# Kernel optimization log

Measured on AMD Instinct MI355X. Metric: run time of the kernel, lower is better.

## Reference

```python
import jax, jax.numpy as jnp
import numpy as np

DIM = 256
NUM_HEADS = 8
REGIONS = [4, 4, 8, 8, 16, 16, 32, 32]  # per-head local window sizes
B, H_IMG, W_IMG = 8, 64, 64


def setup_inputs() -> dict:
    key = jax.random.key(0)
    ks = jax.random.split(key, 6)
    C = DIM
    s = 0.02
    return {
        'x': jax.random.normal(ks[0], (B, H_IMG * W_IMG, C), jnp.float32),
        'Wq': jax.random.normal(ks[1], (C, C), jnp.float32) * s,
        'Wkv': jax.random.normal(ks[2], (C, 2 * C), jnp.float32) * s,
        'Wlkv': jax.random.normal(ks[3], (C, 2 * C), jnp.float32) * s,
        'Wproj': jax.random.normal(ks[4], (C, C), jnp.float32) * s,
        'bproj': jnp.zeros((C,), jnp.float32),
        'H': H_IMG,
        'W': W_IMG,
    }


def _attn(q, k, v, scale):
    # softmax(q k^T * scale) v, batched over leading dims
    a = jax.nn.softmax(jnp.einsum('...qd,...kd->...qk', q, k) * scale, axis=-1)
    return jnp.einsum('...qk,...kd->...qd', a, v)


def reference(x, Wq, Wkv, Wlkv, Wproj, bproj, H, W):
    Bn, N, C = x.shape
    nh = NUM_HEADS
    Ch = C // nh
    scale = Ch ** -0.5
    M = max(REGIONS)

    q = (x @ Wq).reshape(Bn, N, nh, Ch).transpose(0, 2, 1, 3)            # [B,nh,N,Ch]
    kv = (x @ Wkv).reshape(Bn, N, 2, nh, Ch).transpose(2, 0, 3, 1, 4)    # [2,B,nh,N,Ch]
    k, v = kv[0], kv[1]

    head_outs, global_q = [], []
    for i, p in enumerate(REGIONS):
        def patch(a, p=p):  # [B,N,Ch] -> [B,NP,p*p,Ch]
            a = a.reshape(Bn, H // p, p, W // p, p, Ch)
            return a.transpose(0, 1, 3, 2, 4, 5).reshape(Bn, -1, p * p, Ch)
        qp, kp, vp = patch(q[:, i]), patch(k[:, i]), patch(v[:, i])
        # global query: mean over patches -> [B,p,p,Ch], bilinear upsample to [M,M]
        qg = qp.mean(axis=1).reshape(Bn, p, p, Ch)
        if M // p > 1:
            qg = jax.image.resize(qg, (Bn, M, M, Ch), method='bilinear')
        global_q.append(qg.reshape(Bn, M * M, Ch))
        out = _attn(qp, kp, vp, scale)                                    # [B,NP,p*p,Ch]
        head_outs.append(out.reshape(Bn, N, Ch))  # flatten in PATCH order (matches torch code)

    attn_fused = jnp.stack(head_outs, axis=1).transpose(0, 2, 1, 3).reshape(Bn, N, C)
    Q_g = jnp.stack(global_q, axis=1).transpose(0, 2, 1, 3).reshape(Bn, M * M, C)

    # blend: adaptive avg-pool attn_fused to [M,M] (exact pooling since M|H), cross-attend, upsample
    kh, kw = H // M, W // M
    pooled = attn_fused.reshape(Bn, M, kh, M, kw, C).mean(axis=(2, 4)).reshape(Bn, M * M, C)
    kv2 = (pooled @ Wlkv).reshape(Bn, M * M, 2, nh, Ch).transpose(2, 0, 3, 1, 4)
    k2, v2 = kv2[0], kv2[1]
    Qr = Q_g.reshape(Bn, M * M, nh, Ch).transpose(0, 2, 1, 3)             # [B,nh,M^2,Ch]
    gl = _attn(Qr, k2, v2, scale)                                          # [B,nh,M^2,Ch]
    gl = gl.transpose(0, 2, 1, 3).reshape(Bn, M, M, C)
    gl = jax.image.resize(gl, (Bn, H, W, C), method='bilinear').reshape(Bn, N, C)

    return (attn_fused + gl) @ Wproj + bproj
```

## Files before the change

### kernel.cpp

```cpp
#include <hip/hip_runtime.h>
#include <math.h>


typedef __attribute__((ext_vector_type(8))) short bf16x8;
typedef __attribute__((ext_vector_type(4))) short bf16x4;
typedef __attribute__((ext_vector_type(4))) float f32x4;

__device__ inline float bf2f(unsigned short u) {
  union { unsigned int i; float f; } v; v.i = ((unsigned int)u) << 16; return v.f;
}
__device__ inline unsigned short f2bf(float x) {
  union { float f; unsigned int i; } v; v.f = x;
  return (unsigned short)((v.i + 0x7FFFu + ((v.i >> 16) & 1u)) >> 16);
}

__global__ __launch_bounds__(256) void msa_xcast_r13(
    const float* __restrict__ x, unsigned short* __restrict__ xb)
{
  const size_t i = ((size_t)blockIdx.x * 256 + threadIdx.x) * 8;
  const float4 v0 = *reinterpret_cast<const float4*>(&x[i]);
  const float4 v1 = *reinterpret_cast<const float4*>(&x[i + 4]);
  bf16x8 o;
  o[0] = (short)f2bf(v0.x); o[1] = (short)f2bf(v0.y);
  o[2] = (short)f2bf(v0.z); o[3] = (short)f2bf(v0.w);
  o[4] = (short)f2bf(v1.x); o[5] = (short)f2bf(v1.y);
  o[6] = (short)f2bf(v1.z); o[7] = (short)f2bf(v1.w);
  *reinterpret_cast<bf16x8*>(&xb[i]) = o;
}

__global__ __launch_bounds__(256) void msa_wcast_r13(
    const float* __restrict__ Wq, const float* __restrict__ Wkv,
    const float* __restrict__ Wlkv, const float* __restrict__ Wproj,
    unsigned short* __restrict__ Wqkvt, unsigned short* __restrict__ Wlkvt,
    unsigned short* __restrict__ Wprjt)
{
  const int id = blockIdx.x * 256 + threadIdx.x;
  if (id < 196608) {
    const int r = id >> 8, k = id & 255;
    const float v = (r < 256) ? Wq[(size_t)k * 256 + r] : Wkv[(size_t)k * 512 + (r - 256)];
    Wqkvt[id] = f2bf(v);
  } else if (id < 327680) {
    const int j = id - 196608;
    const int n = j >> 8, k = j & 255;
    Wlkvt[j] = f2bf(Wlkv[(size_t)k * 512 + n]);
  } else if (id < 393216) {
    const int j = id - 327680;
    const int n = j >> 8, k = j & 255;
    Wprjt[j] = f2bf(Wproj[(size_t)k * 256 + n]);
  }
}

__global__ __launch_bounds__(256) void msa_gemm_mfma_r13(
    const unsigned short* __restrict__ Ab, const unsigned short* __restrict__ Wt,
    const float* __restrict__ bias, float* __restrict__ Cf,
    unsigned short* __restrict__ Cb, int K, int N)
{
  __shared__ __align__(16) unsigned short A_lds[128][40];
  __shared__ __align__(16) unsigned short B_lds[128][40];

  const int tid = threadIdx.x;
  const int wave = tid >> 6, lane = tid & 63;
  const int l15 = lane & 15, g = lane >> 4;
  const int bm = blockIdx.y * 128, bn = blockIdx.x * 128;
  const int wr = (wave >> 1) * 64, wc = (wave & 1) * 64;

  f32x4 acc[4][4] = {};

  for (int k0 = 0; k0 < K; k0 += 32) {
    __syncthreads();
#pragma unroll
    for (int s = 0; s < 2; ++s) {
      const int id = tid + s * 256;
      const int row = id >> 2, sg = (id & 3) << 3;
      *reinterpret_cast<bf16x8*>(&A_lds[row][sg]) =
          *reinterpret_cast<const bf16x8*>(&Ab[(size_t)(bm + row) * K + k0 + sg]);
      *reinterpret_cast<bf16x8*>(&B_lds[row][sg]) =
          *reinterpret_cast<const bf16x8*>(&Wt[(size_t)(bn + row) * K + k0 + sg]);
    }
    __syncthreads();

    bf16x8 a_frag[4], b_frag[4];
#pragma unroll
    for (int mi = 0; mi < 4; ++mi)
      a_frag[mi] = *reinterpret_cast<const bf16x8*>(&A_lds[wr + mi * 16 + l15][g << 3]);
#pragma unroll
    for (int ni = 0; ni < 4; ++ni)
      b_frag[ni] = *reinterpret_cast<const bf16x8*>(&B_lds[wc + ni * 16 + l15][g << 3]);
#pragma unroll
    for (int mi = 0; mi < 4; ++mi)
#pragma unroll
      for (int ni = 0; ni < 4; ++ni)
        acc[mi][ni] = __builtin_amdgcn_mfma_f32_16x16x32_bf16(
            a_frag[mi], b_frag[ni], acc[mi][ni], 0, 0, 0);
  }

#pragma unroll
  for (int mi = 0; mi < 4; ++mi)
#pragma unroll
    for (int ni = 0; ni < 4; ++ni) {
      const int col = bn + wc + ni * 16 + l15;
#pragma unroll
      for (int i = 0; i < 4; ++i) {
        const int row = bm + wr + mi * 16 + g * 4 + i;
        float v = acc[mi][ni][i];
        if (bias) v += bias[col];
        const size_t idx = (size_t)row * N + col;
        if (Cb) Cb[idx] = f2bf(v); else Cf[idx] = v;
      }
    }
}

__global__ __launch_bounds__(256) void msa_attn_mfma_r13(
    const unsigned short* __restrict__ qsrc, const unsigned short* __restrict__ kvsrc,
    float* __restrict__ outf, unsigned short* __restrict__ outb, int mode)
{
  __shared__ __align__(16) unsigned short K_lds[64][40];
  __shared__ __align__(16) unsigned short V_lds[32][68];

  const int tid = threadIdx.x;
  const int wave = tid >> 6, lane = tid & 63;
  const int q16 = lane & 15, h = lane >> 4;
  const int b = blockIdx.y;

  int head, NTOK, P2, lp, pm1, base, qstr, kvstr, kofs, vofs;
  if (mode) {
    head = blockIdx.z; NTOK = 1024; P2 = 1024; lp = 0; pm1 = 0; base = 0;
    qstr = 256; kvstr = 512; kofs = 0; vofs = 256;
  } else {
    head = 2 + blockIdx.z;
    lp = (head < 4) ? 3 : (head < 6) ? 4 : 5;
    const int p = 1 << lp; pm1 = p - 1;
    NTOK = 4096; P2 = p * p;
    const int patch = (blockIdx.x * 64) >> (2 * lp);
    const int nbp = 64 >> lp;
    const int hb = patch / nbp, wb = patch - (patch / nbp) * nbp;
    base = ((hb << lp)) * 64 + (wb << lp);
    qstr = 768; kvstr = 768; kofs = 256; vofs = 512;
  }
  const int nq = blockIdx.x * 64 + wave * 16 + q16;
  int n;
  if (mode) n = nq;
  else { const int t = nq & (P2 - 1); n = base + ((t >> lp) << 6) + (t & pm1); }

  const bf16x8 qfrag = *reinterpret_cast<const bf16x8*>(
      qsrc + ((size_t)b * NTOK + n) * qstr + head * 32 + 8 * h);

  const float CEXP = 0.25503485947f;
  float l = 0.f;
  f32x4 o0 = {0.f, 0.f, 0.f, 0.f}, o1 = {0.f, 0.f, 0.f, 0.f};
  const f32x4 zc = {0.f, 0.f, 0.f, 0.f};

  const int skey = tid >> 2;
  const int sh = tid & 3;

  for (int kc = 0; kc < P2; kc += 64) {
    __syncthreads();
    {
      const int kk = kc + skey;
      const int nk = mode ? kk : base + ((kk >> lp) << 6) + (kk & pm1);
      const unsigned short* row = kvsrc + ((size_t)b * NTOK + nk) * kvstr + head * 32;
      *reinterpret_cast<bf16x8*>(&K_lds[skey][8 * sh]) =
          *reinterpret_cast<const bf16x8*>(row + kofs + 8 * sh);
      const bf16x8 v = *reinterpret_cast<const bf16x8*>(row + vofs + 8 * sh);
#pragma unroll
      for (int j = 0; j < 8; ++j)
        V_lds[8 * sh + j][skey] = (unsigned short)v[j];
    }
    __syncthreads();

#pragma unroll
    for (int sub = 0; sub < 2; ++sub) {
      const int s32 = sub * 32;
      const bf16x8 k0 = *reinterpret_cast<const bf16x8*>(&K_lds[s32 + q16][8 * h]);
      const bf16x8 k1 = *reinterpret_cast<const bf16x8*>(&K_lds[s32 + 16 + q16][8 * h]);
      const f32x4 st0 = __builtin_amdgcn_mfma_f32_16x16x32_bf16(k0, qfrag, zc, 0, 0, 0);
      const f32x4 st1 = __builtin_amdgcn_mfma_f32_16x16x32_bf16(k1, qfrag, zc, 0, 0, 0);

      bf16x8 pb;
#pragma unroll
      for (int i = 0; i < 4; ++i) {
        const float p0 = exp2f(st0[i] * CEXP);
        const float p1 = exp2f(st1[i] * CEXP);
        l += p0 + p1;
        pb[i] = (short)f2bf(p0);
        pb[4 + i] = (short)f2bf(p1);
      }

      const bf16x4 va0 = *reinterpret_cast<const bf16x4*>(&V_lds[q16][s32 + 4 * h]);
      const bf16x4 vb0 = *reinterpret_cast<const bf16x4*>(&V_lds[q16][s32 + 16 + 4 * h]);
      const bf16x4 va1 = *reinterpret_cast<const bf16x4*>(&V_lds[16 + q16][s32 + 4 * h]);
      const bf16x4 vb1 = *reinterpret_cast<const bf16x4*>(&V_lds[16 + q16][s32 + 16 + 4 * h]);
      bf16x8 v0, v1;
#pragma unroll
      for (int i = 0; i < 4; ++i) {
        v0[i] = va0[i]; v0[4 + i] = vb0[i];
        v1[i] = va1[i]; v1[4 + i] = vb1[i];
      }
      o0 = __builtin_amdgcn_mfma_f32_16x16x32_bf16(v0, pb, o0, 0, 0, 0);
      o1 = __builtin_amdgcn_mfma_f32_16x16x32_bf16(v1, pb, o1, 0, 0, 0);
    }
  }

  l = l + __shfl_xor(l, 16);
  l = l + __shfl_xor(l, 32);
  const float inv = 1.f / l;
  const size_t obase = ((size_t)b * NTOK + nq) * 256 + head * 32;
  if (mode) {
    float* dst = outf + obase;
    float4 w0, w1;
    w0.x = o0[0] * inv; w0.y = o0[1] * inv; w0.z = o0[2] * inv; w0.w = o0[3] * inv;
    w1.x = o1[0] * inv; w1.y = o1[1] * inv; w1.z = o1[2] * inv; w1.w = o1[3] * inv;
    *reinterpret_cast<float4*>(dst + 4 * h) = w0;
    *reinterpret_cast<float4*>(dst + 16 + 4 * h) = w1;
  } else {
    unsigned short* dst = outb + obase;
    uint2 w0, w1;
    w0.x = (unsigned)f2bf(o0[0] * inv) | ((unsigned)f2bf(o0[1] * inv) << 16);
    w0.y = (unsigned)f2bf(o0[2] * inv) | ((unsigned)f2bf(o0[3] * inv) << 16);
    w1.x = (unsigned)f2bf(o1[0] * inv) | ((unsigned)f2bf(o1[1] * inv) << 16);
    w1.y = (unsigned)f2bf(o1[2] * inv) | ((unsigned)f2bf(o1[3] * inv) << 16);
    *reinterpret_cast<uint2*>(dst + 4 * h) = w0;
    *reinterpret_cast<uint2*>(dst + 16 + 4 * h) = w1;
  }
}

__global__ __launch_bounds__(256) void msa_attn_p4_r13(
    const unsigned short* __restrict__ xqkv, unsigned short* __restrict__ out)
{
  const int head = blockIdx.z;
  const int b = blockIdx.y;
  const int nq = blockIdx.x * 256 + threadIdx.x;

  const int patch = nq >> 4;
  const int t = nq & 15;
  const int hb = patch >> 4, wb = patch & 15;
  const int n = (hb * 4 + (t >> 2)) * 64 + (wb * 4 + (t & 3));

  float qr[32];
  {
    const bf16x8* q8 = reinterpret_cast<const bf16x8*>(
        xqkv + ((size_t)b * 4096 + n) * 768 + head * 32);
#pragma unroll
    for (int i = 0; i < 4; ++i) {
      const bf16x8 v = q8[i];
#pragma unroll
      for (int j = 0; j < 8; ++j) qr[i * 8 + j] = bf2f((unsigned short)v[j]);
    }
  }
  const float CEXP = 0.25503485947f;
  float l = 0.f;
  float acc[32] = {};
  const int kbase = (hb * 4) * 64 + wb * 4;
  for (int kk = 0; kk < 16; ++kk) {
    const int nk = kbase + (kk >> 2) * 64 + (kk & 3);
    const unsigned short* rowp = xqkv + ((size_t)b * 4096 + nk) * 768 + head * 32;
    const bf16x8* k8p = reinterpret_cast<const bf16x8*>(rowp + 256);
    const bf16x8* v8p = reinterpret_cast<const bf16x8*>(rowp + 512);
    float s = 0.f;
#pragma unroll
    for (int i = 0; i < 4; ++i) {
      const bf16x8 k8 = k8p[i];
#pragma unroll
      for (int j = 0; j < 8; ++j) s = fmaf(qr[i * 8 + j], bf2f((unsigned short)k8[j]), s);
    }
    const float p = exp2f(s * CEXP);
    l += p;
#pragma unroll
    for (int i = 0; i < 4; ++i) {
      const bf16x8 v8 = v8p[i];
#pragma unroll
      for (int j = 0; j < 8; ++j)
        acc[i * 8 + j] = fmaf(p, bf2f((unsigned short)v8[j]), acc[i * 8 + j]);
    }
  }
  const float inv = 1.f / l;
  unsigned short* dst = out + ((size_t)b * 4096 + nq) * 256 + head * 32;
#pragma unroll
  for (int c = 0; c < 32; ++c) dst[c] = f2bf(acc[c] * inv);
}

__global__ __launch_bounds__(256) void msa_qg_reduce_r13(
    const unsigned short* __restrict__ xqkv, float* __restrict__ qg_all)
{
  __shared__ float red[256];
  const int head = blockIdx.z;
  const int lp = (head < 2) ? 2 : (head < 4) ? 3 : (head < 6) ? 4 : 5;
  const int p = 1 << lp;
  const int P2 = p * p;
  const int nbp = 64 >> lp;
  const int npat = nbp * nbp;
  const int R = (lp <= 3) ? 8 : 1;
  const int total = P2 * 32 * R;
  const int gid = blockIdx.x * 256 + threadIdx.x;
  if (gid >= total) return;
  const int b = blockIdx.y;

  const int c = gid & 31;
  const int tr = gid >> 5;
  const int r = tr & (R - 1);
  const int t = tr >> ((R == 8) ? 3 : 0);
  const int hp = t >> lp, wp = t & (p - 1);

  const unsigned short* src = xqkv + (size_t)b * 4096 * 768 + head * 32 + c;
  float s = 0.f;
  for (int j = r; j < npat; j += R) {
    const int hb = j / nbp, wb = j - (j / nbp) * nbp;
    const int n = ((hb << lp) + hp) * 64 + (wb << lp) + wp;
    s += bf2f(src[(size_t)n * 768]);
  }

  if (R == 8) {
    red[threadIdx.x] = s;
    __syncthreads();
    if (r < 4) red[threadIdx.x] += red[threadIdx.x + 128];
    __syncthreads();
    if (r < 2) red[threadIdx.x] += red[threadIdx.x + 64];
    __syncthreads();
    if (r == 0) {
      s = red[threadIdx.x] + red[threadIdx.x + 32];
      qg_all[((size_t)b * 8 + head) * 32768 + (size_t)t * 32 + c] = s / (float)npat;
    }
  } else {
    qg_all[((size_t)b * 8 + head) * 32768 + (size_t)t * 32 + c] = s / (float)npat;
  }
}

__global__ __launch_bounds__(256) void msa_qg_upsample_r13(
    const float* __restrict__ qg_all, unsigned short* __restrict__ Qg)
{
  const int head = blockIdx.z;
  const int p = (head < 2) ? 4 : (head < 4) ? 8 : (head < 6) ? 16 : 32;
  const int e = blockIdx.x * 256 + threadIdx.x;
  const int b = blockIdx.y;
  const int mlin = e >> 5, c = e & 31;
  const int mi = mlin >> 5, mj = mlin & 31;
  const float* src = qg_all + ((size_t)b * 8 + head) * 32768;
  float v;
  if (p == 32) {
    v = src[(size_t)mlin * 32 + c];
  } else {
    const float s = (float)p / 32.0f;
    const float xf = (mj + 0.5f) * s - 0.5f;
    const float yf = (mi + 0.5f) * s - 0.5f;
    const float xfl = floorf(xf), yfl = floorf(yf);
    const float fx = xf - xfl, fy = yf - yfl;
    const int x0 = (int)xfl, y0 = (int)yfl;
    const int x0c = max(0, min(p - 1, x0)), x1c = max(0, min(p - 1, x0 + 1));
    const int y0c = max(0, min(p - 1, y0)), y1c = max(0, min(p - 1, y0 + 1));
    const float v00 = src[(size_t)(y0c * p + x0c) * 32 + c];
    const float v01 = src[(size_t)(y0c * p + x1c) * 32 + c];
    const float v10 = src[(size_t)(y1c * p + x0c) * 32 + c];
    const float v11 = src[(size_t)(y1c * p + x1c) * 32 + c];
    v = (1.f - fy) * ((1.f - fx) * v00 + fx * v01)
      + fy * ((1.f - fx) * v10 + fx * v11);
  }
  Qg[((size_t)b * 1024 + mlin) * 256 + head * 32 + c] = f2bf(v);
}

__global__ __launch_bounds__(256) void msa_pool_r13(
    const unsigned short* __restrict__ attn, unsigned short* __restrict__ pooled)
{
  const int c = threadIdx.x;
  const int mlin = blockIdx.x;
  const int b = blockIdx.y;
  const int mi = mlin >> 5, mj = mlin & 31;
  const size_t base = (size_t)b * 4096;
  const int r0 = mi * 2, q0 = mj * 2;
  float s = bf2f(attn[(base + (r0 * 64 + q0)) * 256 + c])
          + bf2f(attn[(base + (r0 * 64 + q0 + 1)) * 256 + c])
          + bf2f(attn[(base + ((r0 + 1) * 64 + q0)) * 256 + c])
          + bf2f(attn[(base + ((r0 + 1) * 64 + q0 + 1)) * 256 + c]);
  pooled[((size_t)b * 1024 + mlin) * 256 + c] = f2bf(s * 0.25f);
}

__global__ __launch_bounds__(256) void msa_blend_r13(
    const float* __restrict__ gl, unsigned short* __restrict__ attn)
{
  const int c = threadIdx.x;
  const int n = blockIdx.x;
  const int b = blockIdx.y;
  const int hh = n >> 6, w = n & 63;
  const float xf = (w + 0.5f) * 0.5f - 0.5f;
  const float yf = (hh + 0.5f) * 0.5f - 0.5f;
  const float xfl = floorf(xf), yfl = floorf(yf);
  const float fx = xf - xfl, fy = yf - yfl;
  const int x0 = (int)xfl, y0 = (int)yfl;
  const int x0c = max(0, min(31, x0)), x1c = max(0, min(31, x0 + 1));
  const int y0c = max(0, min(31, y0)), y1c = max(0, min(31, y0 + 1));
  const float* g = gl + (size_t)b * 1024 * 256;
  const float v00 = g[(size_t)(y0c * 32 + x0c) * 256 + c];
  const float v01 = g[(size_t)(y0c * 32 + x1c) * 256 + c];
  const float v10 = g[(size_t)(y1c * 32 + x0c) * 256 + c];
  const float v11 = g[(size_t)(y1c * 32 + x1c) * 256 + c];
  const float v = (1.f - fy) * ((1.f - fx) * v00 + fx * v01)
                + fy * ((1.f - fx) * v10 + fx * v11);
  const size_t idx = ((size_t)b * 4096 + n) * 256 + c;
  attn[idx] = f2bf(bf2f(attn[idx]) + v);
}

extern "C" void kernel_launch(void* const* d_in, const int* in_sizes, int n_in,
                              void* d_out, int out_size, void* d_ws, size_t ws_size,
                              hipStream_t stream)
{
  const float* x     = (const float*)d_in[0];
  const float* Wq    = (const float*)d_in[1];
  const float* Wkv   = (const float*)d_in[2];
  const float* Wlkv  = (const float*)d_in[3];
  const float* Wproj = (const float*)d_in[4];
  const float* bproj = (const float*)d_in[5];

  char* ws = (char*)d_ws;
  unsigned short* xqkv  = (unsigned short*)(ws + 0);
  unsigned short* attnb = (unsigned short*)(ws + 50331648ull);
  unsigned short* Qg    = (unsigned short*)(ws + 67108864ull);
  float* qg_all = (float*)(ws + 71303168ull);
  unsigned short* Wqkvt = (unsigned short*)(ws + 79691776ull);
  unsigned short* Wlkvt = (unsigned short*)(ws + 80084992ull);
  unsigned short* Wprjt = (unsigned short*)(ws + 80347136ull);
  float* gl     = (float*)(ws + 80478208ull);
  unsigned short* xb    = (unsigned short*)(ws + 88866816ull);
  unsigned short* pooled = (unsigned short*)(ws + 0);
  unsigned short* kv2    = (unsigned short*)(ws + 16777216ull);

  msa_xcast_r13<<<dim3(4096), 256, 0, stream>>>(x, xb);
  msa_wcast_r13<<<dim3(1536), 256, 0, stream>>>(Wq, Wkv, Wlkv, Wproj, Wqkvt, Wlkvt, Wprjt);

  msa_gemm_mfma_r13<<<dim3(6, 256), 256, 0, stream>>>(xb, Wqkvt, nullptr, nullptr, xqkv, 256, 768);

  msa_qg_reduce_r13<<<dim3(128, 8, 8), 256, 0, stream>>>(xqkv, qg_all);
  msa_qg_upsample_r13<<<dim3(128, 8, 8), 256, 0, stream>>>(qg_all, Qg);

  msa_attn_p4_r13<<<dim3(16, 8, 2), 256, 0, stream>>>(xqkv, attnb);
  msa_attn_mfma_r13<<<dim3(64, 8, 6), 256, 0, stream>>>(xqkv, xqkv, nullptr, attnb, 0);

  msa_pool_r13<<<dim3(1024, 8), 256, 0, stream>>>(attnb, pooled);
  msa_gemm_mfma_r13<<<dim3(4, 64), 256, 0, stream>>>(pooled, Wlkvt, nullptr, nullptr, kv2, 256, 512);

  msa_attn_mfma_r13<<<dim3(16, 8, 8), 256, 0, stream>>>(Qg, kv2, gl, nullptr, 1);

  msa_blend_r13<<<dim3(4096, 8), 256, 0, stream>>>(gl, attnb);
  msa_gemm_mfma_r13<<<dim3(2, 256), 256, 0, stream>>>(attnb, Wprjt, bproj, (float*)d_out, nullptr, 256, 256);

  (void)in_sizes; (void)n_in; (void)out_size; (void)ws_size;
}
```

Measured before the change: 237.4 us.

## Process four query tiles per wave to reuse K/V fragments in attention

The large-window and global attention kernel now gives each wave 64 queries (four 16-query tiles) instead of 16. Each K/V fragment loaded from LDS feeds four QK and PV MFMA steps, and the grid shrinks fourfold. This cuts LDS staging and global K/V reloads per query. The p=8 heads move to a dedicated single-tile kernel that skips the KV loop. The cost is higher register pressure from four accumulator sets and fewer blocks for the global attention launch (256 blocks), which may lower occupancy.

```diff
diff --git a/kernel.cpp b/kernel.cpp
--- a/kernel.cpp
+++ b/kernel.cpp
@@ -14,7 +14,7 @@
   return (unsigned short)((v.i + 0x7FFFu + ((v.i >> 16) & 1u)) >> 16);
 }
 
-__global__ __launch_bounds__(256) void msa_xcast_r13(
+__global__ __launch_bounds__(256) void msa_xcast_r15(
     const float* __restrict__ x, unsigned short* __restrict__ xb)
 {
   const size_t i = ((size_t)blockIdx.x * 256 + threadIdx.x) * 8;
@@ -28,7 +28,7 @@
   *reinterpret_cast<bf16x8*>(&xb[i]) = o;
 }
 
-__global__ __launch_bounds__(256) void msa_wcast_r13(
+__global__ __launch_bounds__(256) void msa_wcast_r15(
     const float* __restrict__ Wq, const float* __restrict__ Wkv,
     const float* __restrict__ Wlkv, const float* __restrict__ Wproj,
     unsigned short* __restrict__ Wqkvt, unsigned short* __restrict__ Wlkvt,
@@ -50,7 +50,7 @@
   }
 }
 
-__global__ __launch_bounds__(256) void msa_gemm_mfma_r13(
+__global__ __launch_bounds__(256) void msa_gemm_mfma_r15(
     const unsigned short* __restrict__ Ab, const unsigned short* __restrict__ Wt,
     const float* __restrict__ bias, float* __restrict__ Cf,
     unsigned short* __restrict__ Cb, int K, int N)
@@ -110,7 +110,33 @@
     }
 }
 
-__global__ __launch_bounds__(256) void msa_attn_mfma_r13(
+__device__ inline void tile_step_r15(
+    const bf16x8 k0, const bf16x8 k1, const bf16x8 v0, const bf16x8 v1,
+    const bf16x8 qf, float& l, f32x4& o0, f32x4& o1)
+{
+  const f32x4 zc = {0.f, 0.f, 0.f, 0.f};
+  const float CEXP = 0.25503485947f;
+  const f32x4 st0 = __builtin_amdgcn_mfma_f32_16x16x32_bf16(k0, qf, zc, 0, 0, 0);
+  const f32x4 st1 = __builtin_amdgcn_mfma_f32_16x16x32_bf16(k1, qf, zc, 0, 0, 0);
+  const float e00 = exp2f(st0[0] * CEXP);
+  const float e01 = exp2f(st0[1] * CEXP);
+  const float e02 = exp2f(st0[2] * CEXP);
+  const float e03 = exp2f(st0[3] * CEXP);
+  const float e10 = exp2f(st1[0] * CEXP);
+  const float e11 = exp2f(st1[1] * CEXP);
+  const float e12 = exp2f(st1[2] * CEXP);
+  const float e13 = exp2f(st1[3] * CEXP);
+  l += ((e00 + e01) + (e02 + e03)) + ((e10 + e11) + (e12 + e13));
+  bf16x8 pb;
+  pb[0] = (short)f2bf(e00); pb[1] = (short)f2bf(e01);
+  pb[2] = (short)f2bf(e02); pb[3] = (short)f2bf(e03);
+  pb[4] = (short)f2bf(e10); pb[5] = (short)f2bf(e11);
+  pb[6] = (short)f2bf(e12); pb[7] = (short)f2bf(e13);
+  o0 = __builtin_amdgcn_mfma_f32_16x16x32_bf16(v0, pb, o0, 0, 0, 0);
+  o1 = __builtin_amdgcn_mfma_f32_16x16x32_bf16(v1, pb, o1, 0, 0, 0);
+}
+
+__global__ __launch_bounds__(256) void msa_attn_big_r15(
     const unsigned short* __restrict__ qsrc, const unsigned short* __restrict__ kvsrc,
     float* __restrict__ outf, unsigned short* __restrict__ outb, int mode)
 {
@@ -127,28 +153,37 @@
     head = blockIdx.z; NTOK = 1024; P2 = 1024; lp = 0; pm1 = 0; base = 0;
     qstr = 256; kvstr = 512; kofs = 0; vofs = 256;
   } else {
-    head = 2 + blockIdx.z;
-    lp = (head < 4) ? 3 : (head < 6) ? 4 : 5;
+    head = 4 + blockIdx.z;
+    lp = (head < 6) ? 4 : 5;
     const int p = 1 << lp; pm1 = p - 1;
     NTOK = 4096; P2 = p * p;
-    const int patch = (blockIdx.x * 64) >> (2 * lp);
+    const int patch = (blockIdx.x * 256) >> (2 * lp);
     const int nbp = 64 >> lp;
     const int hb = patch / nbp, wb = patch - (patch / nbp) * nbp;
     base = ((hb << lp)) * 64 + (wb << lp);
     qstr = 768; kvstr = 768; kofs = 256; vofs = 512;
   }
-  const int nq = blockIdx.x * 64 + wave * 16 + q16;
-  int n;
-  if (mode) n = nq;
-  else { const int t = nq & (P2 - 1); n = base + ((t >> lp) << 6) + (t & pm1); }
-
-  const bf16x8 qfrag = *reinterpret_cast<const bf16x8*>(
-      qsrc + ((size_t)b * NTOK + n) * qstr + head * 32 + 8 * h);
-
-  const float CEXP = 0.25503485947f;
-  float l = 0.f;
-  f32x4 o0 = {0.f, 0.f, 0.f, 0.f}, o1 = {0.f, 0.f, 0.f, 0.f};
-  const f32x4 zc = {0.f, 0.f, 0.f, 0.f};
+  const int q0 = blockIdx.x * 256 + wave * 64;
+  const int nqA = q0 + q16, nqB = q0 + 16 + q16, nqC = q0 + 32 + q16, nqD = q0 + 48 + q16;
+
+  bf16x8 qfA, qfB, qfC, qfD;
+  {
+    int n;
+    if (mode) n = nqA; else { const int tt = nqA & (P2 - 1); n = base + ((tt >> lp) << 6) + (tt & pm1); }
+    qfA = *reinterpret_cast<const bf16x8*>(qsrc + ((size_t)b * NTOK + n) * qstr + head * 32 + 8 * h);
+    if (mode) n = nqB; else { const int tt = nqB & (P2 - 1); n = base + ((tt >> lp) << 6) + (tt & pm1); }
+    qfB = *reinterpret_cast<const bf16x8*>(qsrc + ((size_t)b * NTOK + n) * qstr + head * 32 + 8 * h);
+    if (mode) n = nqC; else { const int tt = nqC & (P2 - 1); n = base + ((tt >> lp) << 6) + (tt & pm1); }
+    qfC = *reinterpret_cast<const bf16x8*>(qsrc + ((size_t)b * NTOK + n) * qstr + head * 32 + 8 * h);
+    if (mode) n = nqD; else { const int tt = nqD & (P2 - 1); n = base + ((tt >> lp) << 6) + (tt & pm1); }
+    qfD = *reinterpret_cast<const bf16x8*>(qsrc + ((size_t)b * NTOK + n) * qstr + head * 32 + 8 * h);
+  }
+
+  float lA = 0.f, lB = 0.f, lC = 0.f, lD = 0.f;
+  f32x4 o0A = {0.f,0.f,0.f,0.f}, o1A = {0.f,0.f,0.f,0.f};
+  f32x4 o0B = {0.f,0.f,0.f,0.f}, o1B = {0.f,0.f,0.f,0.f};
+  f32x4 o0C = {0.f,0.f,0.f,0.f}, o1C = {0.f,0.f,0.f,0.f};
+  f32x4 o0D = {0.f,0.f,0.f,0.f}, o1D = {0.f,0.f,0.f,0.f};
 
   const int skey = tid >> 2;
   const int sh = tid & 3;
@@ -173,19 +208,6 @@
       const int s32 = sub * 32;
       const bf16x8 k0 = *reinterpret_cast<const bf16x8*>(&K_lds[s32 + q16][8 * h]);
       const bf16x8 k1 = *reinterpret_cast<const bf16x8*>(&K_lds[s32 + 16 + q16][8 * h]);
-      const f32x4 st0 = __builtin_amdgcn_mfma_f32_16x16x32_bf16(k0, qfrag, zc, 0, 0, 0);
-      const f32x4 st1 = __builtin_amdgcn_mfma_f32_16x16x32_bf16(k1, qfrag, zc, 0, 0, 0);
-
-      bf16x8 pb;
-#pragma unroll
-      for (int i = 0; i < 4; ++i) {
-        const float p0 = exp2f(st0[i] * CEXP);
-        const float p1 = exp2f(st1[i] * CEXP);
-        l += p0 + p1;
-        pb[i] = (short)f2bf(p0);
-        pb[4 + i] = (short)f2bf(p1);
-      }
-
       const bf16x4 va0 = *reinterpret_cast<const bf16x4*>(&V_lds[q16][s32 + 4 * h]);
       const bf16x4 vb0 = *reinterpret_cast<const bf16x4*>(&V_lds[q16][s32 + 16 + 4 * h]);
       const bf16x4 va1 = *reinterpret_cast<const bf16x4*>(&V_lds[16 + q16][s32 + 4 * h]);
@@ -196,35 +218,141 @@
         v0[i] = va0[i]; v0[4 + i] = vb0[i];
         v1[i] = va1[i]; v1[4 + i] = vb1[i];
       }
-      o0 = __builtin_amdgcn_mfma_f32_16x16x32_bf16(v0, pb, o0, 0, 0, 0);
-      o1 = __builtin_amdgcn_mfma_f32_16x16x32_bf16(v1, pb, o1, 0, 0, 0);
-    }
+      tile_step_r15(k0, k1, v0, v1, qfA, lA, o0A, o1A);
+      tile_step_r15(k0, k1, v0, v1, qfB, lB, o0B, o1B);
+      tile_step_r15(k0, k1, v0, v1, qfC, lC, o0C, o1C);
+      tile_step_r15(k0, k1, v0, v1, qfD, lD, o0D, o1D);
+    }
+  }
+
+#define R15_EPI(LT, O0, O1, NQ)                                                \
+  {                                                                            \
+    float lt = LT;                                                             \
+    lt = lt + __shfl_xor(lt, 16);                                              \
+    lt = lt + __shfl_xor(lt, 32);                                              \
+    const float inv = 1.f / lt;                                                \
+    const size_t obase = ((size_t)b * NTOK + (NQ)) * 256 + head * 32;          \
+    if (mode) {                                                                \
+      float* dst = outf + obase;                                               \
+      float4 w0, w1;                                                           \
+      w0.x = O0[0] * inv; w0.y = O0[1] * inv;                                  \
+      w0.z = O0[2] * inv; w0.w = O0[3] * inv;                                  \
+      w1.x = O1[0] * inv; w1.y = O1[1] * inv;                                  \
+      w1.z = O1[2] * inv; w1.w = O1[3] * inv;                                  \
+      *reinterpret_cast<float4*>(dst + 4 * h) = w0;                            \
+      *reinterpret_cast<float4*>(dst + 16 + 4 * h) = w1;                       \
+    } else {                                                                   \
+      unsigned short* dst = outb + obase;                                      \
+      uint2 w0, w1;                                                            \
+      w0.x = (unsigned)f2bf(O0[0] * inv) | ((unsigned)f2bf(O0[1] * inv) << 16);\
+      w0.y = (unsigned)f2bf(O0[2] * inv) | ((unsigned)f2bf(O0[3] * inv) << 16);\
+      w1.x = (unsigned)f2bf(O1[0] * inv) | ((unsigned)f2bf(O1[1] * inv) << 16);\
+      w1.y = (unsigned)f2bf(O1[2] * inv) | ((unsigned)f2bf(O1[3] * inv) << 16);\
+      *reinterpret_cast<uint2*>(dst + 4 * h) = w0;                             \
+      *reinterpret_cast<uint2*>(dst + 16 + 4 * h) = w1;                        \
+    }                                                                          \
+  }
+
+  R15_EPI(lA, o0A, o1A, nqA)
+  R15_EPI(lB, o0B, o1B, nqB)
+  R15_EPI(lC, o0C, o1C, nqC)
+  R15_EPI(lD, o0D, o1D, nqD)
+#undef R15_EPI
+}
+
+__global__ __launch_bounds__(256) void msa_attn_mid_r15(
+    const unsigned short* __restrict__ kvsrc, unsigned short* __restrict__ outb)
+{
+  __shared__ __align__(16) unsigned short K_lds[64][40];
+  __shared__ __align__(16) unsigned short V_lds[32][68];
+
+  const int tid = threadIdx.x;
+  const int wave = tid >> 6, lane = tid & 63;
+  const int q16 = lane & 15, h = lane >> 4;
+  const int b = blockIdx.y;
+
+  const int head = 2 + blockIdx.z;
+  const int lp = 3, pm1 = 7;
+  const int P2 = 64;
+  const int patch = blockIdx.x;
+  const int nbp = 8;
+  const int hb = patch / nbp, wb = patch - (patch / nbp) * nbp;
+  const int base = ((hb << lp)) * 64 + (wb << lp);
+
+  const int nq = blockIdx.x * 64 + wave * 16 + q16;
+  const int t = nq & (P2 - 1);
+  const int n = base + ((t >> lp) << 6) + (t & pm1);
+
+  const bf16x8 qfrag = *reinterpret_cast<const bf16x8*>(
+      kvsrc + ((size_t)b * 4096 + n) * 768 + head * 32 + 8 * h);
+
+  const float CEXP = 0.25503485947f;
+  float l = 0.f;
+  f32x4 o0 = {0.f, 0.f, 0.f, 0.f}, o1 = {0.f, 0.f, 0.f, 0.f};
+  const f32x4 zc = {0.f, 0.f, 0.f, 0.f};
+
+  const int skey = tid >> 2;
+  const int sh = tid & 3;
+  {
+    const int nk = base + ((skey >> lp) << 6) + (skey & pm1);
+    const unsigned short* row = kvsrc + ((size_t)b * 4096 + nk) * 768 + head * 32;
+    *reinterpret_cast<bf16x8*>(&K_lds[skey][8 * sh]) =
+        *reinterpret_cast<const bf16x8*>(row + 256 + 8 * sh);
+    const bf16x8 v = *reinterpret_cast<const bf16x8*>(row + 512 + 8 * sh);
+#pragma unroll
+    for (int j = 0; j < 8; ++j)
+      V_lds[8 * sh + j][skey] = (unsigned short)v[j];
+  }
+  __syncthreads();
+
+#pragma unroll
+  for (int sub = 0; sub < 2; ++sub) {
+    const int s32 = sub * 32;
+    const bf16x8 k0 = *reinterpret_cast<const bf16x8*>(&K_lds[s32 + q16][8 * h]);
+    const bf16x8 k1 = *reinterpret_cast<const bf16x8*>(&K_lds[s32 + 16 + q16][8 * h]);
+    const f32x4 st0 = __builtin_amdgcn_mfma_f32_16x16x32_bf16(k0, qfrag, zc, 0, 0, 0);
+    const f32x4 st1 = __builtin_amdgcn_mfma_f32_16x16x32_bf16(k1, qfrag, zc, 0, 0, 0);
+    float e0[4], e1[4];
+#pragma unroll
+    for (int i = 0; i < 4; ++i) {
+      e0[i] = exp2f(st0[i] * CEXP);
+      e1[i] = exp2f(st1[i] * CEXP);
+    }
+    l += ((e0[0] + e0[1]) + (e0[2] + e0[3])) + ((e1[0] + e1[1]) + (e1[2] + e1[3]));
+    bf16x8 pb;
+#pragma unroll
+    for (int i = 0; i < 4; ++i) {
+      pb[i] = (short)f2bf(e0[i]);
+      pb[4 + i] = (short)f2bf(e1[i]);
+    }
+    const bf16x4 va0 = *reinterpret_cast<const bf16x4*>(&V_lds[q16][s32 + 4 * h]);
+    const bf16x4 vb0 = *reinterpret_cast<const bf16x4*>(&V_lds[q16][s32 + 16 + 4 * h]);
+    const bf16x4 va1 = *reinterpret_cast<const bf16x4*>(&V_lds[16 + q16][s32 + 4 * h]);
+    const bf16x4 vb1 = *reinterpret_cast<const bf16x4*>(&V_lds[16 + q16][s32 + 16 + 4 * h]);
+    bf16x8 v0, v1;
+#pragma unroll
+    for (int i = 0; i < 4; ++i) {
+      v0[i] = va0[i]; v0[4 + i] = vb0[i];
+      v1[i] = va1[i]; v1[4 + i] = vb1[i];
+    }
+    o0 = __builtin_amdgcn_mfma_f32_16x16x32_bf16(v0, pb, o0, 0, 0, 0);
+    o1 = __builtin_amdgcn_mfma_f32_16x16x32_bf16(v1, pb, o1, 0, 0, 0);
   }
 
   l = l + __shfl_xor(l, 16);
   l = l + __shfl_xor(l, 32);
   const float inv = 1.f / l;
-  const size_t obase = ((size_t)b * NTOK + nq) * 256 + head * 32;
-  if (mode) {
-    float* dst = outf + obase;
-    float4 w0, w1;
-    w0.x = o0[0] * inv; w0.y = o0[1] * inv; w0.z = o0[2] * inv; w0.w = o0[3] * inv;
-    w1.x = o1[0] * inv; w1.y = o1[1] * inv; w1.z = o1[2] * inv; w1.w = o1[3] * inv;
-    *reinterpret_cast<float4*>(dst + 4 * h) = w0;
-    *reinterpret_cast<float4*>(dst + 16 + 4 * h) = w1;
-  } else {
-    unsigned short* dst = outb + obase;
-    uint2 w0, w1;
-    w0.x = (unsigned)f2bf(o0[0] * inv) | ((unsigned)f2bf(o0[1] * inv) << 16);
-    w0.y = (unsigned)f2bf(o0[2] * inv) | ((unsigned)f2bf(o0[3] * inv) << 16);
-    w1.x = (unsigned)f2bf(o1[0] * inv) | ((unsigned)f2bf(o1[1] * inv) << 16);
-    w1.y = (unsigned)f2bf(o1[2] * inv) | ((unsigned)f2bf(o1[3] * inv) << 16);
-    *reinterpret_cast<uint2*>(dst + 4 * h) = w0;
-    *reinterpret_cast<uint2*>(dst + 16 + 4 * h) = w1;
-  }
-}
-
-__global__ __launch_bounds__(256) void msa_attn_p4_r13(
+  unsigned short* dst = outb + ((size_t)b * 4096 + nq) * 256 + head * 32;
+  uint2 w0, w1;
+  w0.x = (unsigned)f2bf(o0[0] * inv) | ((unsigned)f2bf(o0[1] * inv) << 16);
+  w0.y = (unsigned)f2bf(o0[2] * inv) | ((unsigned)f2bf(o0[3] * inv) << 16);
+  w1.x = (unsigned)f2bf(o1[0] * inv) | ((unsigned)f2bf(o1[1] * inv) << 16);
+  w1.y = (unsigned)f2bf(o1[2] * inv) | ((unsigned)f2bf(o1[3] * inv) << 16);
+  *reinterpret_cast<uint2*>(dst + 4 * h) = w0;
+  *reinterpret_cast<uint2*>(dst + 16 + 4 * h) = w1;
+}
+
+__global__ __launch_bounds__(256) void msa_attn_p4_r15(
     const unsigned short* __restrict__ xqkv, unsigned short* __restrict__ out)
 {
   const int head = blockIdx.z;
@@ -279,7 +407,7 @@
   for (int c = 0; c < 32; ++c) dst[c] = f2bf(acc[c] * inv);
 }
 
-__global__ __launch_bounds__(256) void msa_qg_reduce_r13(
+__global__ __launch_bounds__(256) void msa_qg_reduce_r15(
     const unsigned short* __restrict__ xqkv, float* __restrict__ qg_all)
 {
   __shared__ float red[256];
@@ -325,7 +453,7 @@
   }
 }
 
-__global__ __launch_bounds__(256) void msa_qg_upsample_r13(
+__global__ __launch_bounds__(256) void msa_qg_upsample_r15(
     const float* __restrict__ qg_all, unsigned short* __restrict__ Qg)
 {
   const int head = blockIdx.z;
@@ -357,7 +485,7 @@
   Qg[((size_t)b * 1024 + mlin) * 256 + head * 32 + c] = f2bf(v);
 }
 
-__global__ __launch_bounds__(256) void msa_pool_r13(
+__global__ __launch_bounds__(256) void msa_pool_r15(
     const unsigned short* __restrict__ attn, unsigned short* __restrict__ pooled)
 {
   const int c = threadIdx.x;
@@ -373,7 +501,7 @@
   pooled[((size_t)b * 1024 + mlin) * 256 + c] = f2bf(s * 0.25f);
 }
 
-__global__ __launch_bounds__(256) void msa_blend_r13(
+__global__ __launch_bounds__(256) void msa_blend_r15(
     const float* __restrict__ gl, unsigned short* __restrict__ attn)
 {
   const int c = threadIdx.x;
@@ -422,24 +550,25 @@
   unsigned short* pooled = (unsigned short*)(ws + 0);
   unsigned short* kv2    = (unsigned short*)(ws + 16777216ull);
 
-  msa_xcast_r13<<<dim3(4096), 256, 0, stream>>>(x, xb);
-  msa_wcast_r13<<<dim3(1536), 256, 0, stream>>>(Wq, Wkv, Wlkv, Wproj, Wqkvt, Wlkvt, Wprjt);
-
-  msa_gemm_mfma_r13<<<dim3(6, 256), 256, 0, stream>>>(xb, Wqkvt, nullptr, nullptr, xqkv, 256, 768);
-
-  msa_qg_reduce_r13<<<dim3(128, 8, 8), 256, 0, stream>>>(xqkv, qg_all);
-  msa_qg_upsample_r13<<<dim3(128, 8, 8), 256, 0, stream>>>(qg_all, Qg);
-
-  msa_attn_p4_r13<<<dim3(16, 8, 2), 256, 0, stream>>>(xqkv, attnb);
-  msa_attn_mfma_r13<<<dim3(64, 8, 6), 256, 0, stream>>>(xqkv, xqkv, nullptr, attnb, 0);
-
-  msa_pool_r13<<<dim3(1024, 8), 256, 0, stream>>>(attnb, pooled);
-  msa_gemm_mfma_r13<<<dim3(4, 64), 256, 0, stream>>>(pooled, Wlkvt, nullptr, nullptr, kv2, 256, 512);
-
-  msa_attn_mfma_r13<<<dim3(16, 8, 8), 256, 0, stream>>>(Qg, kv2, gl, nullptr, 1);
-
-  msa_blend_r13<<<dim3(4096, 8), 256, 0, stream>>>(gl, attnb);
-  msa_gemm_mfma_r13<<<dim3(2, 256), 256, 0, stream>>>(attnb, Wprjt, bproj, (float*)d_out, nullptr, 256, 256);
+  msa_xcast_r15<<<dim3(4096), 256, 0, stream>>>(x, xb);
+  msa_wcast_r15<<<dim3(1536), 256, 0, stream>>>(Wq, Wkv, Wlkv, Wproj, Wqkvt, Wlkvt, Wprjt);
+
+  msa_gemm_mfma_r15<<<dim3(6, 256), 256, 0, stream>>>(xb, Wqkvt, nullptr, nullptr, xqkv, 256, 768);
+
+  msa_qg_reduce_r15<<<dim3(128, 8, 8), 256, 0, stream>>>(xqkv, qg_all);
+  msa_qg_upsample_r15<<<dim3(128, 8, 8), 256, 0, stream>>>(qg_all, Qg);
+
+  msa_attn_p4_r15<<<dim3(16, 8, 2), 256, 0, stream>>>(xqkv, attnb);
+  msa_attn_mid_r15<<<dim3(64, 8, 2), 256, 0, stream>>>(xqkv, attnb);
+  msa_attn_big_r15<<<dim3(16, 8, 4), 256, 0, stream>>>(xqkv, xqkv, nullptr, attnb, 0);
+
+  msa_pool_r15<<<dim3(1024, 8), 256, 0, stream>>>(attnb, pooled);
+  msa_gemm_mfma_r15<<<dim3(4, 64), 256, 0, stream>>>(pooled, Wlkvt, nullptr, nullptr, kv2, 256, 512);
+
+  msa_attn_big_r15<<<dim3(4, 8, 8), 256, 0, stream>>>(Qg, kv2, gl, nullptr, 1);
+
+  msa_blend_r15<<<dim3(4096, 8), 256, 0, stream>>>(gl, attnb);
+  msa_gemm_mfma_r15<<<dim3(2, 256), 256, 0, stream>>>(attnb, Wprjt, bproj, (float*)d_out, nullptr, 256, 256);
 
   (void)in_sizes; (void)n_in; (void)out_size; (void)ws_size;
 }
```

New measurement: 238.5 us. About the same (+0.4%).
